# Performance work log

Measured on AMD Instinct MI355X. Metric: run time of the kernel, lower is better.

Reference implementation:

```python
import jax, jax.numpy as jnp
import numpy as np
from jax import lax

NUM_SEG = 64
EPS = 1e-12

def conv2d(x, w, b=None):
    y = lax.conv_general_dilated(x, w, (1, 1), 'SAME', dimension_numbers=('NCHW', 'OIHW', 'NCHW'))
    if b is not None:
        y = y + b[None, :, None, None]
    return y

def layer_norm_chw(x):
    # LayerNorm over (C,H,W) per sample, no affine
    mu = x.mean(axis=(1, 2, 3), keepdims=True)
    var = jnp.mean((x - mu) ** 2, axis=(1, 2, 3), keepdims=True)
    return (x - mu) / jnp.sqrt(var + EPS)

def spade(x, sem_rs, w_sh, b_sh, w_g, b_g, w_be, b_be):
    xn = layer_norm_chw(x)
    h = jax.nn.relu(conv2d(sem_rs, w_sh, b_sh))
    gamma = conv2d(h, w_g, b_g)
    beta = conv2d(h, w_be, b_be)
    return xn * (1.0 + gamma) + beta

def painted_semantic_map(f_sem, segmap):
    # f_sem: [B,C,Hp,Wp] float; segmap: [B,Hi,Wi] int
    B, C, Hp, Wp = f_sem.shape
    _, Hi, Wi = segmap.shape
    # torch nearest interpolate: src = floor(dst * in/out)
    rows = (jnp.arange(Hp) * Hi) // Hp
    cols = (jnp.arange(Wp) * Wi) // Wp
    seg_small = segmap[:, rows[:, None], cols[None, :]]  # [B,Hp,Wp]
    flat_feat = f_sem.transpose(0, 2, 3, 1).reshape(-1, C)  # [B*Hp*Wp, C]
    bidx = jnp.repeat(jnp.arange(B), Hp * Wp)
    gid = bidx * NUM_SEG + jnp.clip(seg_small.reshape(-1), 0, NUM_SEG - 1)
    sums = jax.ops.segment_sum(flat_feat, gid, num_segments=B * NUM_SEG)
    cnts = jax.ops.segment_sum(jnp.ones((flat_feat.shape[0],), flat_feat.dtype), gid, num_segments=B * NUM_SEG)
    # scatter_mean + nan_to_num: empty segments -> 0
    avg = jnp.where(cnts[:, None] > 0, sums / jnp.maximum(cnts, 1.0)[:, None], 0.0)
    pid = jnp.repeat(jnp.arange(B), Hi * Wi) * NUM_SEG + jnp.clip(segmap.reshape(-1), 0, NUM_SEG - 1)
    return avg[pid].reshape(B, Hi, Wi, C).transpose(0, 3, 1, 2)  # [B,C,Hi,Wi]

def setup_inputs() -> dict:
    key = jax.random.key(0)
    ks = jax.random.split(key, 32)
    B, Cm, Cs, Hp, Wp, Hi, Wi, Hm = 2, 1536, 384, 32, 32, 448, 448, 128
    d = {}
    d['x_main'] = jax.random.normal(ks[0], (B, Cm, Hp, Wp), jnp.float32)
    d['f_semantic'] = jax.random.normal(ks[1], (B, Cs, Hp, Wp), jnp.float32)
    s = 0.02
    d['w_sh0'] = jax.random.normal(ks[2], (Hm, Cs, 3, 3), jnp.float32) * s
    d['b_sh0'] = jax.random.normal(ks[3], (Hm,), jnp.float32) * s
    d['w_g0'] = jax.random.normal(ks[4], (Cm, Hm, 3, 3), jnp.float32) * s
    d['b_g0'] = jax.random.normal(ks[5], (Cm,), jnp.float32) * s
    d['w_be0'] = jax.random.normal(ks[6], (Cm, Hm, 3, 3), jnp.float32) * s
    d['b_be0'] = jax.random.normal(ks[7], (Cm,), jnp.float32) * s
    d['w_sh1'] = jax.random.normal(ks[8], (Hm, Cs, 3, 3), jnp.float32) * s
    d['b_sh1'] = jax.random.normal(ks[9], (Hm,), jnp.float32) * s
    d['w_g1'] = jax.random.normal(ks[10], (8, Hm, 3, 3), jnp.float32) * s
    d['b_g1'] = jax.random.normal(ks[11], (8,), jnp.float32) * s
    d['w_be1'] = jax.random.normal(ks[12], (8, Hm, 3, 3), jnp.float32) * s
    d['b_be1'] = jax.random.normal(ks[13], (8,), jnp.float32) * s
    d['w_sh2'] = jax.random.normal(ks[14], (Hm, Cs, 3, 3), jnp.float32) * s
    d['b_sh2'] = jax.random.normal(ks[15], (Hm,), jnp.float32) * s
    d['w_g2'] = jax.random.normal(ks[16], (16, Hm, 3, 3), jnp.float32) * s
    d['b_g2'] = jax.random.normal(ks[17], (16,), jnp.float32) * s
    d['w_be2'] = jax.random.normal(ks[18], (16, Hm, 3, 3), jnp.float32) * s
    d['b_be2'] = jax.random.normal(ks[19], (16,), jnp.float32) * s
    d['w_c0'] = jax.random.normal(ks[20], (8, Cm, 1, 1), jnp.float32) * s
    d['bias0'] = jax.random.normal(ks[21], (8,), jnp.float32) * s
    d['w_c1'] = jax.random.normal(ks[22], (16, 8, 1, 1), jnp.float32) * s
    d['bias1'] = jax.random.normal(ks[23], (16,), jnp.float32) * s
    d['w_c2'] = jax.random.normal(ks[24], (1, 16, 1, 1), jnp.float32) * s
    d['bias2'] = jax.random.normal(ks[25], (1,), jnp.float32) * s
    d['segmap'] = jax.random.randint(ks[26], (B, Hi, Wi), 0, NUM_SEG, jnp.int32)
    return d

def reference(x_main, f_semantic, w_sh0, b_sh0, w_g0, b_g0, w_be0, b_be0,
              w_sh1, b_sh1, w_g1, b_g1, w_be1, b_be1,
              w_sh2, b_sh2, w_g2, b_g2, w_be2, b_be2,
              w_c0, bias0, w_c1, bias1, w_c2, bias2, segmap):
    B, Cm, Hp, Wp = x_main.shape
    pm = painted_semantic_map(f_semantic, segmap)  # [B,Cs,Hi,Wi]
    # bilinear (align_corners=False) resize to main-path resolution; identical at all 3 SPADE layers
    sem_rs = jax.image.resize(pm, (B, pm.shape[1], Hp, Wp), method='bilinear')
    h = spade(x_main, sem_rs, w_sh0, b_sh0, w_g0, b_g0, w_be0, b_be0)
    h = jax.nn.softplus(conv2d(h, w_c0) + bias0[None, :, None, None])
    h = spade(h, sem_rs, w_sh1, b_sh1, w_g1, b_g1, w_be1, b_be1)
    h = jax.nn.softplus(conv2d(h, w_c1) + bias1[None, :, None, None])
    h = spade(h, sem_rs, w_sh2, b_sh2, w_g2, b_g2, w_be2, b_be2)
    h = jax.nn.softplus(conv2d(h, w_c2) + bias2[None, :, None, None])
    return h
```

## Files before the change

### kernel.cpp

```cpp
#include <hip/hip_runtime.h>
#include <hip/hip_bf16.h>

#define DEV __device__ __forceinline__

constexpr int B = 2;
constexpr int CM = 1536;
constexpr int CS = 384;
constexpr int HP = 32, WP = 32, P = 1024;
constexpr int HI = 448, WI = 448;
constexpr int HM = 128;
constexpr int NSEG = 64;

constexpr size_t OFF_AVG  = 0;
constexpr size_t OFF_SEMT = 49152;
constexpr size_t OFF_HSHT = 835584;
constexpr size_t OFF_OUT0 = 1622016;
constexpr size_t OFF_P6   = 4767744;
constexpr size_t OFF_H1A  = 5160960;
constexpr size_t OFF_OUT1 = 5177344;
constexpr size_t OFF_H2A  = 5193728;
constexpr size_t OFF_OUT2 = 5226496;
constexpr size_t OFF_STATS= 5259264;
constexpr size_t OFF_PACK = 5259280;

constexpr size_t PK0 = 0;
constexpr size_t PK1 = 1327104;
constexpr size_t PK2 = 4866048;
constexpr size_t PK3 = 4902912;
constexpr int    PK_CHUNKS = 617472;

typedef __attribute__((ext_vector_type(8))) short s16x8;
typedef __attribute__((ext_vector_type(4))) float f32x4;

DEV float softplus_f(float x) {
    return fmaxf(x, 0.f) + log1pf(expf(-fabsf(x)));
}
DEV ushort f2bf(float f) {
    union { float f; unsigned u; } x; x.f = f;
    unsigned r = x.u + 0x7fffu + ((x.u >> 16) & 1u);
    return (ushort)(r >> 16);
}
DEV float bf2f(ushort u) {
    union { unsigned u; float f; } x; x.u = ((unsigned)u) << 16;
    return x.f;
}

__global__ __launch_bounds__(256) void k_seg_avg(const float* __restrict__ f_sem,
                                                 const int* __restrict__ segmap,
                                                 float* __restrict__ ws) {
    int b = blockIdx.y;
    int c0 = blockIdx.x * 8;
    __shared__ int   segs[P];
    __shared__ float sums[NSEG][9];
    __shared__ float cnt[NSEG];
    int t = threadIdx.x;
    for (int i = t; i < NSEG * 9; i += 256) (&sums[0][0])[i] = 0.f;
    if (t < NSEG) cnt[t] = 0.f;
    __syncthreads();
    for (int p = t; p < P; p += 256) {
        int i = p >> 5, j = p & 31;
        int s = segmap[(b * HI + i * 14) * WI + j * 14];
        s = min(max(s, 0), NSEG - 1);
        segs[p] = s;
        atomicAdd(&cnt[s], 1.f);
    }
    __syncthreads();
    #pragma unroll
    for (int ch = 0; ch < 8; ++ch) {
        const float* fp = f_sem + ((size_t)b * CS + c0 + ch) * P;
        #pragma unroll
        for (int pb = 0; pb < 4; ++pb) {
            int p = pb * 256 + t;
            float v = fp[p];
            atomicAdd(&sums[segs[p]][ch], v);
        }
    }
    __syncthreads();
    for (int i = t; i < NSEG * 8; i += 256) {
        int s = i >> 3, ch = i & 7;
        float cv = cnt[s];
        ws[OFF_AVG + ((size_t)(b * NSEG + s)) * CS + c0 + ch] =
            cv > 0.f ? sums[s][ch] / cv : 0.f;
    }
}

__global__ __launch_bounds__(256) void k_paint(const int* __restrict__ segmap,
                                               float* __restrict__ ws) {
    int oxt = blockIdx.x, oy = blockIdx.y, b = blockIdx.z;
    int ox0 = oxt * 8;
    __shared__ float WbT[8][65];
    __shared__ float norm[8];
    int t = threadIdx.x;
    for (int i = t; i < 8 * 65; i += 256) (&WbT[0][0])[i] = 0.f;
    __syncthreads();

    float cy = 14.f * oy + 6.5f;
    int y0 = 14 * oy - 7;
    int x0 = 14 * ox0 - 7;
    for (int k = t; k < 28 * 126; k += 256) {
        int r = k / 126, cix = k % 126;
        int jy = y0 + r, jx = x0 + cix;
        if (jy < 0 || jy >= HI || jx < 0 || jx >= WI) continue;
        float wy = 1.f - fabsf(cy - (float)jy) * (1.f / 14.f);
        int s = segmap[(b * HI + jy) * WI + jx];
        s = min(max(s, 0), NSEG - 1);
        int oxhi = (jx + 7) / 14;
        #pragma unroll
        for (int d = 0; d < 2; ++d) {
            int ox = oxhi - d;
            if (ox < ox0 || ox >= ox0 + 8) continue;
            float wx = 1.f - fabsf(14.f * ox + 6.5f - (float)jx) * (1.f / 14.f);
            if (wx > 0.f) atomicAdd(&WbT[ox - ox0][s], wy * wx);
        }
    }
    __syncthreads();
    if (t < 8) {
        float sm = 0.f;
        #pragma unroll
        for (int s = 0; s < NSEG; ++s) sm += WbT[t][s];
        norm[t] = 1.f / sm;
    }
    __syncthreads();

    const float* ap0 = ws + OFF_AVG + (size_t)b * NSEG * CS;
    for (int c = t; c < CS; c += 256) {
        float acc[8] = {};
        const float* ap = ap0 + c;
        #pragma unroll
        for (int s = 0; s < NSEG; ++s) {
            float a = ap[(size_t)s * CS];
            #pragma unroll
            for (int ox = 0; ox < 8; ++ox) acc[ox] += WbT[ox][s] * a;
        }
        #pragma unroll
        for (int ox = 0; ox < 8; ++ox) {
            int op = oy * 32 + ox0 + ox;
            ws[OFF_SEMT + ((size_t)b * P + op) * CS + c] = acc[ox] * norm[ox];
        }
    }
}

__global__ __launch_bounds__(256) void k_ln0_stats(const float* __restrict__ x,
                                                   float* __restrict__ stats) {
    int b = blockIdx.y;
    const float4* xp = (const float4*)(x + (size_t)b * CM * P);
    int n4 = CM * P / 4;
    float s = 0.f, q = 0.f;
    for (int i = blockIdx.x * 256 + threadIdx.x; i < n4; i += 64 * 256) {
        float4 v = xp[i];
        s += v.x + v.y + v.z + v.w;
        q += v.x * v.x + v.y * v.y + v.z * v.z + v.w * v.w;
    }
    for (int o = 32; o > 0; o >>= 1) { s += __shfl_down(s, o); q += __shfl_down(q, o); }
    __shared__ float ls[4], lq[4];
    int w = threadIdx.x >> 6;
    if ((threadIdx.x & 63) == 0) { ls[w] = s; lq[w] = q; }
    __syncthreads();
    if (threadIdx.x == 0) {
        atomicAdd(&stats[b * 2],     ls[0] + ls[1] + ls[2] + ls[3]);
        atomicAdd(&stats[b * 2 + 1], lq[0] + lq[1] + lq[2] + lq[3]);
    }
}

__global__ __launch_bounds__(256) void k_wpack(
    const float* __restrict__ w_sh0, const float* __restrict__ w_sh1, const float* __restrict__ w_sh2,
    const float* __restrict__ w_g0,  const float* __restrict__ w_be0,
    const float* __restrict__ w_g1,  const float* __restrict__ w_be1,
    const float* __restrict__ w_g2,  const float* __restrict__ w_be2,
    ushort* __restrict__ packU)
{
    for (int c8 = blockIdx.x * 256 + threadIdx.x; c8 < PK_CHUNKS; c8 += gridDim.x * 256) {
        size_t e = (size_t)c8 * 8;
        const float* s0 = nullptr;
        bool zero = false;
        if (e < PK1) {
            size_t r = e;
            int ci0 = (int)(r & 31), co2 = (int)((r >> 5) & 31);
            int tap = (int)((r >> 10) % 9);
            int kct = (int)((r / 9216) % 12), ct = (int)(r / 110592);
            int coG = ct * 32 + co2, sel = coG >> 7, cow = coG & 127;
            const float* wp = sel == 0 ? w_sh0 : (sel == 1 ? w_sh1 : w_sh2);
            s0 = &wp[((size_t)cow * CS + kct * 32 + ci0) * 9 + tap];
        } else if (e < PK2) {
            size_t r = e - PK1;
            int ci0 = (int)(r & 31), co2 = (int)((r >> 5) & 31);
            int tap = (int)((r >> 10) % 9);
            int kct = (int)((r / 9216) % 4), ct = (int)(r / 36864);
            int cog = ct * 16 + (co2 & 15);
            const float* wp = co2 < 16 ? w_g0 : w_be0;
            s0 = &wp[((size_t)cog * HM + kct * 32 + ci0) * 9 + tap];
        } else if (e < PK3) {
            size_t r = e - PK2;
            int ci0 = (int)(r & 31), co2 = (int)((r >> 5) & 31);
            int tap = (int)((r >> 10) % 9);
            int kct = (int)(r / 9216);
            zero = ((co2 & 15) >= 8);
            int cog = co2 & 7;
            const float* wp = co2 < 16 ? w_g1 : w_be1;
            if (!zero) s0 = &wp[((size_t)cog * HM + kct * 32 + ci0) * 9 + tap];
        } else {
            size_t r = e - PK3;
            int ci0 = (int)(r & 31), co2 = (int)((r >> 5) & 31);
            int tap = (int)((r >> 10) % 9);
            int kct = (int)(r / 9216);
            int cog = co2 & 15;
            const float* wp = co2 < 16 ? w_g2 : w_be2;
            s0 = &wp[((size_t)cog * HM + kct * 32 + ci0) * 9 + tap];
        }
        s16x8 o;
        #pragma unroll
        for (int i = 0; i < 8; ++i) {
            float v = zero ? 0.f : s0[(size_t)i * 9];
            o[i] = (short)f2bf(v);
        }
        *(s16x8*)&packU[e] = o;
    }
}

template<int MODE>
__global__ __launch_bounds__(256) void k_conv_mfma(
    const float* __restrict__ semT, const ushort* __restrict__ hshTin,
    const ushort* __restrict__ packW,
    const float* __restrict__ bb0, const float* __restrict__ bb1, const float* __restrict__ bb2,
    const float* __restrict__ xsrc, const float* __restrict__ st, float Ninv,
    float* __restrict__ outF, ushort* __restrict__ outH)
{
    constexpr int ROWS = (MODE == 0) ? 4 : 8;
    constexpr int NT   = ROWS / 2;
    constexpr int XR   = ROWS + 2;
    constexpr int KTOT = (MODE == 0) ? 12 : 4;
    constexpr int CBASE = (MODE == 2) ? 128 : (MODE == 3) ? 256 : 0;
    constexpr int NP = (MODE == 1) ? 1536 : (MODE == 2) ? 8 : 16;

    int pt = blockIdx.x, ctile = blockIdx.y;
    int zz = blockIdx.z;
    int b  = (MODE == 0) ? (zz % B) : zz;
    int ks = (MODE == 0) ? (zz / B) : 0;
    int t = threadIdx.x, l = t & 63, wv = t >> 6;
    int y0 = pt * ROWS;

    __shared__ __align__(16) ushort Wl[9][32][40];
    __shared__ __align__(16) ushort Xl[XR][34][40];

    f32x4 acc[2][NT] = {};

    for (int kc = 0; kc < 128; kc += 32) {
        __syncthreads();
        for (int j = t; j < XR * 34 * 4; j += 256) {
            int slot = j >> 2, part = j & 3;
            int r = slot / 34, c = slot % 34;
            int gy = y0 - 1 + r, gx = c - 1;
            s16x8 v = {};
            if (gy >= 0 && gy < HP && gx >= 0 && gx < WP) {
                int pix = gy * WP + gx;
                if constexpr (MODE == 0) {
                    const float4* sp = (const float4*)&semT[((size_t)b * P + pix) * CS + ks * 128 + kc + part * 8];
                    float4 x0 = sp[0], x1 = sp[1];
                    v[0] = (short)f2bf(x0.x); v[1] = (short)f2bf(x0.y);
                    v[2] = (short)f2bf(x0.z); v[3] = (short)f2bf(x0.w);
                    v[4] = (short)f2bf(x1.x); v[5] = (short)f2bf(x1.y);
                    v[6] = (short)f2bf(x1.z); v[7] = (short)f2bf(x1.w);
                } else {
                    v = *(const s16x8*)&hshTin[((size_t)b * P + pix) * 384 + CBASE + kc + part * 8];
                }
            }
            *(s16x8*)&Xl[r][c][part * 8] = v;
        }
        const ushort* wsrc = packW + (size_t)(ctile * KTOT + ks * 4 + (kc >> 5)) * 9216;
        for (int j = t; j < 1152; j += 256) {
            int tap = j >> 7, co2 = (j >> 2) & 31, part = j & 3;
            *(s16x8*)&Wl[tap][co2][part * 8] = *(const s16x8*)&wsrc[(size_t)j * 8];
        }
        __syncthreads();
        #pragma unroll
        for (int tap = 0; tap < 9; ++tap) {
            int dy = tap / 3, dx = tap % 3;
            s16x8 a0 = *(const s16x8*)&Wl[tap][l & 15][(l >> 4) * 8];
            s16x8 a1 = *(const s16x8*)&Wl[tap][16 + (l & 15)][(l >> 4) * 8];
            #pragma unroll
            for (int nt = 0; nt < NT; ++nt) {
                int q = wv * (16 * NT) + nt * 16 + (l & 15);
                int ry = (q >> 5) + dy, rx = (q & 31) + dx;
                s16x8 bf = *(const s16x8*)&Xl[ry][rx][(l >> 4) * 8];
                acc[0][nt] = __builtin_amdgcn_mfma_f32_16x16x32_bf16(a0, bf, acc[0][nt], 0, 0, 0);
                acc[1][nt] = __builtin_amdgcn_mfma_f32_16x16x32_bf16(a1, bf, acc[1][nt], 0, 0, 0);
            }
        }
    }

    if constexpr (MODE == 0) {
        __syncthreads();
        ushort (*T)[36] = (ushort(*)[36])(&Xl[0][0][0]);
        #pragma unroll
        for (int mt = 0; mt < 2; ++mt)
            #pragma unroll
            for (int nt = 0; nt < NT; ++nt)
                #pragma unroll
                for (int r = 0; r < 4; ++r) {
                    int m = mt * 16 + (l >> 4) * 4 + r;
                    int pl = wv * (16 * NT) + nt * 16 + (l & 15);
                    T[pl][m] = f2bf(acc[mt][nt][r]);
                }
        __syncthreads();
        int row = t >> 1, half = t & 1;
        ushort* dst = outH + ((size_t)((ks * B + b) * P) + pt * 128 + row) * 384 + ctile * 32 + half * 16;
        *(s16x8*)dst = *(const s16x8*)&T[row][half * 16];
    } else {
        float mu = st[b * 2] * Ninv;
        float var = st[b * 2 + 1] * Ninv - mu * mu;
        float rs = rsqrtf(var + 1e-12f);
        #pragma unroll
        for (int nt = 0; nt < NT; ++nt)
            #pragma unroll
            for (int r = 0; r < 4; ++r) {
                int m = (l >> 4) * 4 + r;
                if (MODE == 2 && m >= 8) continue;
                int cog = (MODE == 1) ? ctile * 16 + m : m;
                int px = pt * 256 + wv * 64 + nt * 16 + (l & 15);
                float gam = acc[0][nt][r] + bb0[cog];
                float bet = acc[1][nt][r] + bb1[cog];
                float xv = xsrc[((size_t)b * NP + cog) * P + px];
                outF[((size_t)b * NP + cog) * P + px] = (xv - mu) * rs * (1.f + gam) + bet;
            }
    }
}

__global__ __launch_bounds__(256) void k_hsh_fin(const ushort* __restrict__ part,
                                                 const float* __restrict__ b0,
                                                 const float* __restrict__ b1,
                                                 const float* __restrict__ b2,
                                                 ushort* __restrict__ hsh) {
    int gid = blockIdx.x * 256 + threadIdx.x;
    int grp = gid % 48, pixg = gid / 48;
    int ch0 = grp * 8;
    size_t base = (size_t)pixg * 384 + ch0;
    s16x8 p0 = *(const s16x8*)&part[(size_t)0 * B * P * 384 + base];
    s16x8 p1 = *(const s16x8*)&part[(size_t)1 * B * P * 384 + base];
    s16x8 p2 = *(const s16x8*)&part[(size_t)2 * B * P * 384 + base];
    int sel = ch0 >> 7;
    const float* bp = sel == 0 ? b0 : (sel == 1 ? b1 : b2);
    int cb = ch0 & 127;
    s16x8 o;
    #pragma unroll
    for (int i = 0; i < 8; ++i) {
        float v = bf2f((ushort)p0[i]) + bf2f((ushort)p1[i]) + bf2f((ushort)p2[i]) + bp[cb + i];
        o[i] = (short)f2bf(fmaxf(v, 0.f));
    }
    *(s16x8*)&hsh[base] = o;
}

__global__ __launch_bounds__(256) void k_c1x1_a(const float* __restrict__ out0,
                                                const float* __restrict__ w,
                                                float* __restrict__ part) {
    int b = blockIdx.z, ks = blockIdx.y, pg = blockIdx.x;
    int t = threadIdx.x, lp = t & 63, g = t >> 6;
    int pix = pg * 64 + lp;
    float acc[8] = {};
    int ci0 = ks * 64 + g * 16;
    for (int i = 0; i < 16; i++) {
        int ci = ci0 + i;
        float v = out0[((size_t)b * CM + ci) * P + pix];
        #pragma unroll
        for (int o = 0; o < 8; o++) acc[o] += w[o * CM + ci] * v;
    }
    __shared__ float red[4][64][8];
    #pragma unroll
    for (int o = 0; o < 8; o++) red[g][lp][o] = acc[o];
    __syncthreads();
    for (int idx = t; idx < 512; idx += 256) {
        int pp = idx >> 3, o = idx & 7;
        float s = red[0][pp][o] + red[1][pp][o] + red[2][pp][o] + red[3][pp][o];
        part[(((size_t)b * 24 + ks) * 8 + o) * P + pg * 64 + pp] = s;
    }
}

__global__ __launch_bounds__(256) void k_c1x1_a_fin(const float* __restrict__ part,
                                                    const float* __restrict__ bias,
                                                    float* __restrict__ h1a,
                                                    float* __restrict__ stats) {
    int b = blockIdx.y, t = threadIdx.x;
    int idx = blockIdx.x * 1024 + t;
    float s = 0.f, q = 0.f;
    for (int k = 0; k < 4; ++k, idx += 256) {
        int o = idx >> 10, pix = idx & 1023;
        float v = 0.f;
        for (int ks = 0; ks < 24; ks++) v += part[(((size_t)b * 24 + ks) * 8 + o) * P + pix];
        v += bias[o];
        v = softplus_f(v);
        h1a[((size_t)b * 8 + o) * P + pix] = v;
        s += v; q += v * v;
    }
    for (int o2 = 32; o2 > 0; o2 >>= 1) { s += __shfl_down(s, o2); q += __shfl_down(q, o2); }
    __shared__ float ls[4], lq[4];
    int w = t >> 6;
    if ((t & 63) == 0) { ls[w] = s; lq[w] = q; }
    __syncthreads();
    if (t == 0) {
        atomicAdd(&stats[(B + b) * 2],     ls[0] + ls[1] + ls[2] + ls[3]);
        atomicAdd(&stats[(B + b) * 2 + 1], lq[0] + lq[1] + lq[2] + lq[3]);
    }
}

__global__ __launch_bounds__(256) void k_c1x1_b(const float* __restrict__ out1,
                                                const float* __restrict__ w,
                                                const float* __restrict__ bias,
                                                float* __restrict__ h2a,
                                                float* __restrict__ stats) {
    int b = blockIdx.y, t = threadIdx.x;
    int pix = blockIdx.x * 256 + t;
    float vin[8];
    #pragma unroll
    for (int ci = 0; ci < 8; ci++) vin[ci] = out1[((size_t)b * 8 + ci) * P + pix];
    float s = 0.f, q = 0.f;
    #pragma unroll
    for (int o = 0; o < 16; o++) {
        float a = bias[o];
        #pragma unroll
        for (int ci = 0; ci < 8; ci++) a += w[o * 8 + ci] * vin[ci];
        a = softplus_f(a);
        h2a[((size_t)b * 16 + o) * P + pix] = a;
        s += a; q += a * a;
    }
    for (int o2 = 32; o2 > 0; o2 >>= 1) { s += __shfl_down(s, o2); q += __shfl_down(q, o2); }
    __shared__ float ls[4], lq[4];
    int w2 = t >> 6;
    if ((t & 63) == 0) { ls[w2] = s; lq[w2] = q; }
    __syncthreads();
    if (t == 0) {
        atomicAdd(&stats[(2 * B + b) * 2],     ls[0] + ls[1] + ls[2] + ls[3]);
        atomicAdd(&stats[(2 * B + b) * 2 + 1], lq[0] + lq[1] + lq[2] + lq[3]);
    }
}

__global__ __launch_bounds__(256) void k_final(const float* __restrict__ out2,
                                               const float* __restrict__ w,
                                               const float* __restrict__ bias,
                                               float* __restrict__ out) {
    int b = blockIdx.y, t = threadIdx.x;
    int pix = blockIdx.x * 256 + t;
    float a = bias[0];
    #pragma unroll
    for (int ci = 0; ci < 16; ci++) a += w[ci] * out2[((size_t)b * 16 + ci) * P + pix];
    a = softplus_f(a);
    out[(size_t)b * P + pix] = a;
}

extern "C" void kernel_launch(void* const* d_in, const int* in_sizes, int n_in,
                              void* d_out, int out_size, void* d_ws, size_t ws_size,
                              hipStream_t stream) {
    const float* x_main = (const float*)d_in[0];
    const float* f_sem  = (const float*)d_in[1];
    const float* w_sh0 = (const float*)d_in[2];  const float* b_sh0 = (const float*)d_in[3];
    const float* w_g0  = (const float*)d_in[4];  const float* b_g0  = (const float*)d_in[5];
    const float* w_be0 = (const float*)d_in[6];  const float* b_be0 = (const float*)d_in[7];
    const float* w_sh1 = (const float*)d_in[8];  const float* b_sh1 = (const float*)d_in[9];
    const float* w_g1  = (const float*)d_in[10]; const float* b_g1  = (const float*)d_in[11];
    const float* w_be1 = (const float*)d_in[12]; const float* b_be1 = (const float*)d_in[13];
    const float* w_sh2 = (const float*)d_in[14]; const float* b_sh2 = (const float*)d_in[15];
    const float* w_g2  = (const float*)d_in[16]; const float* b_g2  = (const float*)d_in[17];
    const float* w_be2 = (const float*)d_in[18]; const float* b_be2 = (const float*)d_in[19];
    const float* w_c0  = (const float*)d_in[20]; const float* bias0 = (const float*)d_in[21];
    const float* w_c1  = (const float*)d_in[22]; const float* bias1 = (const float*)d_in[23];
    const float* w_c2  = (const float*)d_in[24]; const float* bias2 = (const float*)d_in[25];
    const int*   segmap = (const int*)d_in[26];

    float* ws = (float*)d_ws;
    float* out = (float*)d_out;
    float* stats = ws + OFF_STATS;
    ushort* hshU = (ushort*)(ws + OFF_HSHT);
    ushort* partU = (ushort*)(ws + OFF_OUT0);
    ushort* packU = (ushort*)(ws + OFF_PACK);

    hipMemsetAsync((void*)stats, 0, 16 * sizeof(float), stream);

    k_wpack<<<dim3(2412), 256, 0, stream>>>(w_sh0, w_sh1, w_sh2, w_g0, w_be0,
                                            w_g1, w_be1, w_g2, w_be2, packU);
    k_seg_avg<<<dim3(48, B), 256, 0, stream>>>(f_sem, segmap, ws);
    k_ln0_stats<<<dim3(64, B), 256, 0, stream>>>(x_main, stats);
    k_paint<<<dim3(4, 32, B), 256, 0, stream>>>(segmap, ws);

    k_conv_mfma<0><<<dim3(8, 12, 3 * B), 256, 0, stream>>>(
        ws + OFF_SEMT, nullptr, packU + PK0,
        nullptr, nullptr, nullptr, nullptr, nullptr, 0.f, nullptr, partU);
    k_hsh_fin<<<dim3(384), 256, 0, stream>>>(partU, b_sh0, b_sh1, b_sh2, hshU);

    k_conv_mfma<1><<<dim3(4, 96, B), 256, 0, stream>>>(
        nullptr, hshU, packU + PK1,
        b_g0, b_be0, nullptr, x_main, stats, 1.f / (float)(CM * P),
        ws + OFF_OUT0, nullptr);

    k_c1x1_a<<<dim3(16, 24, B), 256, 0, stream>>>(ws + OFF_OUT0, w_c0, ws + OFF_P6);
    k_c1x1_a_fin<<<dim3(8, B), 256, 0, stream>>>(ws + OFF_P6, bias0, ws + OFF_H1A, stats);

    k_conv_mfma<2><<<dim3(4, 1, B), 256, 0, stream>>>(
        nullptr, hshU, packU + PK2,
        b_g1, b_be1, nullptr, ws + OFF_H1A, stats + 2 * B, 1.f / (float)(8 * P),
        ws + OFF_OUT1, nullptr);

    k_c1x1_b<<<dim3(4, B), 256, 0, stream>>>(ws + OFF_OUT1, w_c1, bias1, ws + OFF_H2A, stats);

    k_conv_mfma<3><<<dim3(4, 1, B), 256, 0, stream>>>(
        nullptr, hshU, packU + PK3,
        b_g2, b_be2, nullptr, ws + OFF_H2A, stats + 4 * B, 1.f / (float)(16 * P),
        ws + OFF_OUT2, nullptr);

    k_final<<<dim3(4, B), 256, 0, stream>>>(ws + OFF_OUT2, w_c2, bias2, out);
}
```

Measured before the change: 319.4 us.

## Fuse 1x1 convs and softplus into SPADE conv epilogues

The SPADE-modulated output of each stage is no longer written to global memory. Instead, each conv kernel's epilogue applies the following 1x1 convolution directly. For stage 0, each channel tile writes per-tile partial sums of the 8 output channels, and a new finisher kernel reduces the 96 partials and applies softplus and the layer-norm stats. Stages 1 and 2 do their 1x1 conv, softplus and stats in-block through shared memory, which removes three kernel launches and the large fp32 intermediate round trip, at the cost of more epilogue work and a larger partial buffer.

```diff
diff --git a/kernel.cpp b/kernel.cpp
--- a/kernel.cpp
+++ b/kernel.cpp
@@ -221,9 +221,11 @@
 __global__ __launch_bounds__(256) void k_conv_mfma(
     const float* __restrict__ semT, const ushort* __restrict__ hshTin,
     const ushort* __restrict__ packW,
-    const float* __restrict__ bb0, const float* __restrict__ bb1, const float* __restrict__ bb2,
+    const float* __restrict__ bb0, const float* __restrict__ bb1,
     const float* __restrict__ xsrc, const float* __restrict__ st, float Ninv,
-    float* __restrict__ outF, ushort* __restrict__ outH)
+    const float* __restrict__ wcf, const float* __restrict__ bcf,
+    float* __restrict__ fout, float* __restrict__ statsOut,
+    ushort* __restrict__ outH)
 {
     constexpr int ROWS = (MODE == 0) ? 4 : 8;
     constexpr int NT   = ROWS / 2;
@@ -305,23 +307,104 @@
         int row = t >> 1, half = t & 1;
         ushort* dst = outH + ((size_t)((ks * B + b) * P) + pt * 128 + row) * 384 + ctile * 32 + half * 16;
         *(s16x8*)dst = *(const s16x8*)&T[row][half * 16];
+    } else if constexpr (MODE == 1) {
+        float mu = st[b * 2] * Ninv;
+        float var = st[b * 2 + 1] * Ninv - mu * mu;
+        float rs = rsqrtf(var + 1e-12f);
+        __syncthreads();
+        float (*WC)[17] = (float(*)[17])(&Wl[0][0][0]);
+        if (t < 128) WC[t >> 4][t & 15] = wcf[(size_t)(t >> 4) * CM + ctile * 16 + (t & 15)];
+        __syncthreads();
+        float pacc[8][4] = {};
+        #pragma unroll
+        for (int nt = 0; nt < NT; ++nt)
+            #pragma unroll
+            for (int r = 0; r < 4; ++r) {
+                int m = (l >> 4) * 4 + r;
+                int cog = ctile * 16 + m;
+                int px = pt * 256 + wv * 64 + nt * 16 + (l & 15);
+                float gam = acc[0][nt][r] + bb0[cog];
+                float bet = acc[1][nt][r] + bb1[cog];
+                float xv = xsrc[((size_t)b * NP + cog) * P + px];
+                float o0 = (xv - mu) * rs * (1.f + gam) + bet;
+                #pragma unroll
+                for (int o = 0; o < 8; ++o) pacc[o][nt] += WC[o][m] * o0;
+            }
+        #pragma unroll
+        for (int o = 0; o < 8; ++o)
+            #pragma unroll
+            for (int nt = 0; nt < NT; ++nt) {
+                float v = pacc[o][nt];
+                v += __shfl_xor(v, 16);
+                v += __shfl_xor(v, 32);
+                if ((l >> 4) == 0)
+                    fout[(((size_t)b * 96 + ctile) * 8 + o) * P + pt * 256 + wv * 64 + nt * 16 + l] = v;
+            }
+    } else if constexpr (MODE == 2) {
+        float mu = st[b * 2] * Ninv;
+        float var = st[b * 2 + 1] * Ninv - mu * mu;
+        float rs = rsqrtf(var + 1e-12f);
+        __syncthreads();
+        float (*O1)[9] = (float(*)[9])(&Xl[0][0][0]);
+        #pragma unroll
+        for (int nt = 0; nt < NT; ++nt)
+            #pragma unroll
+            for (int r = 0; r < 4; ++r) {
+                int m = (l >> 4) * 4 + r;
+                if (m < 8) {
+                    int pxl = wv * 64 + nt * 16 + (l & 15);
+                    int px = pt * 256 + pxl;
+                    float gam = acc[0][nt][r] + bb0[m];
+                    float bet = acc[1][nt][r] + bb1[m];
+                    float xv = xsrc[((size_t)b * NP + m) * P + px];
+                    O1[pxl][m] = (xv - mu) * rs * (1.f + gam) + bet;
+                }
+            }
+        __syncthreads();
+        float vin[8];
+        #pragma unroll
+        for (int ci = 0; ci < 8; ++ci) vin[ci] = O1[t][ci];
+        float s = 0.f, q = 0.f;
+        #pragma unroll
+        for (int o = 0; o < 16; ++o) {
+            float a = bcf[o];
+            #pragma unroll
+            for (int ci = 0; ci < 8; ++ci) a += wcf[o * 8 + ci] * vin[ci];
+            a = softplus_f(a);
+            fout[((size_t)b * 16 + o) * P + pt * 256 + t] = a;
+            s += a; q += a * a;
+        }
+        for (int o2 = 32; o2 > 0; o2 >>= 1) { s += __shfl_down(s, o2); q += __shfl_down(q, o2); }
+        float* red = (float*)&Wl[0][0][0];
+        if ((t & 63) == 0) { red[wv] = s; red[4 + wv] = q; }
+        __syncthreads();
+        if (t == 0) {
+            atomicAdd(&statsOut[b * 2],     red[0] + red[1] + red[2] + red[3]);
+            atomicAdd(&statsOut[b * 2 + 1], red[4] + red[5] + red[6] + red[7]);
+        }
     } else {
         float mu = st[b * 2] * Ninv;
         float var = st[b * 2 + 1] * Ninv - mu * mu;
         float rs = rsqrtf(var + 1e-12f);
+        __syncthreads();
+        float (*O2)[17] = (float(*)[17])(&Xl[0][0][0]);
         #pragma unroll
         for (int nt = 0; nt < NT; ++nt)
             #pragma unroll
             for (int r = 0; r < 4; ++r) {
                 int m = (l >> 4) * 4 + r;
-                if (MODE == 2 && m >= 8) continue;
-                int cog = (MODE == 1) ? ctile * 16 + m : m;
-                int px = pt * 256 + wv * 64 + nt * 16 + (l & 15);
-                float gam = acc[0][nt][r] + bb0[cog];
-                float bet = acc[1][nt][r] + bb1[cog];
-                float xv = xsrc[((size_t)b * NP + cog) * P + px];
-                outF[((size_t)b * NP + cog) * P + px] = (xv - mu) * rs * (1.f + gam) + bet;
+                int pxl = wv * 64 + nt * 16 + (l & 15);
+                int px = pt * 256 + pxl;
+                float gam = acc[0][nt][r] + bb0[m];
+                float bet = acc[1][nt][r] + bb1[m];
+                float xv = xsrc[((size_t)b * NP + m) * P + px];
+                O2[pxl][m] = (xv - mu) * rs * (1.f + gam) + bet;
             }
+        __syncthreads();
+        float a = bcf[0];
+        #pragma unroll
+        for (int ci = 0; ci < 16; ++ci) a += wcf[ci] * O2[t][ci];
+        fout[(size_t)b * P + pt * 256 + t] = softplus_f(a);
     }
 }
 
@@ -349,47 +432,21 @@
     *(s16x8*)&hsh[base] = o;
 }
 
-__global__ __launch_bounds__(256) void k_c1x1_a(const float* __restrict__ out0,
-                                                const float* __restrict__ w,
-                                                float* __restrict__ part) {
-    int b = blockIdx.z, ks = blockIdx.y, pg = blockIdx.x;
-    int t = threadIdx.x, lp = t & 63, g = t >> 6;
-    int pix = pg * 64 + lp;
-    float acc[8] = {};
-    int ci0 = ks * 64 + g * 16;
-    for (int i = 0; i < 16; i++) {
-        int ci = ci0 + i;
-        float v = out0[((size_t)b * CM + ci) * P + pix];
-        #pragma unroll
-        for (int o = 0; o < 8; o++) acc[o] += w[o * CM + ci] * v;
-    }
-    __shared__ float red[4][64][8];
-    #pragma unroll
-    for (int o = 0; o < 8; o++) red[g][lp][o] = acc[o];
-    __syncthreads();
-    for (int idx = t; idx < 512; idx += 256) {
-        int pp = idx >> 3, o = idx & 7;
-        float s = red[0][pp][o] + red[1][pp][o] + red[2][pp][o] + red[3][pp][o];
-        part[(((size_t)b * 24 + ks) * 8 + o) * P + pg * 64 + pp] = s;
-    }
-}
-
-__global__ __launch_bounds__(256) void k_c1x1_a_fin(const float* __restrict__ part,
-                                                    const float* __restrict__ bias,
-                                                    float* __restrict__ h1a,
-                                                    float* __restrict__ stats) {
+__global__ __launch_bounds__(256) void k_c1a_fin(const float* __restrict__ part,
+                                                 const float* __restrict__ bias,
+                                                 float* __restrict__ h1a,
+                                                 float* __restrict__ stats) {
     int b = blockIdx.y, t = threadIdx.x;
-    int idx = blockIdx.x * 1024 + t;
-    float s = 0.f, q = 0.f;
-    for (int k = 0; k < 4; ++k, idx += 256) {
-        int o = idx >> 10, pix = idx & 1023;
-        float v = 0.f;
-        for (int ks = 0; ks < 24; ks++) v += part[(((size_t)b * 24 + ks) * 8 + o) * P + pix];
-        v += bias[o];
-        v = softplus_f(v);
-        h1a[((size_t)b * 8 + o) * P + pix] = v;
-        s += v; q += v * v;
-    }
+    int idx = blockIdx.x * 256 + t;
+    int o = idx >> 10, pix = idx & 1023;
+    float v = 0.f;
+    #pragma unroll 8
+    for (int ct = 0; ct < 96; ++ct)
+        v += part[(((size_t)b * 96 + ct) * 8 + o) * P + pix];
+    v += bias[o];
+    v = softplus_f(v);
+    h1a[((size_t)b * 8 + o) * P + pix] = v;
+    float s = v, q = v * v;
     for (int o2 = 32; o2 > 0; o2 >>= 1) { s += __shfl_down(s, o2); q += __shfl_down(q, o2); }
     __shared__ float ls[4], lq[4];
     int w = t >> 6;
@@ -399,50 +456,6 @@
         atomicAdd(&stats[(B + b) * 2],     ls[0] + ls[1] + ls[2] + ls[3]);
         atomicAdd(&stats[(B + b) * 2 + 1], lq[0] + lq[1] + lq[2] + lq[3]);
     }
-}
-
-__global__ __launch_bounds__(256) void k_c1x1_b(const float* __restrict__ out1,
-                                                const float* __restrict__ w,
-                                                const float* __restrict__ bias,
-                                                float* __restrict__ h2a,
-                                                float* __restrict__ stats) {
-    int b = blockIdx.y, t = threadIdx.x;
-    int pix = blockIdx.x * 256 + t;
-    float vin[8];
-    #pragma unroll
-    for (int ci = 0; ci < 8; ci++) vin[ci] = out1[((size_t)b * 8 + ci) * P + pix];
-    float s = 0.f, q = 0.f;
-    #pragma unroll
-    for (int o = 0; o < 16; o++) {
-        float a = bias[o];
-        #pragma unroll
-        for (int ci = 0; ci < 8; ci++) a += w[o * 8 + ci] * vin[ci];
-        a = softplus_f(a);
-        h2a[((size_t)b * 16 + o) * P + pix] = a;
-        s += a; q += a * a;
-    }
-    for (int o2 = 32; o2 > 0; o2 >>= 1) { s += __shfl_down(s, o2); q += __shfl_down(q, o2); }
-    __shared__ float ls[4], lq[4];
-    int w2 = t >> 6;
-    if ((t & 63) == 0) { ls[w2] = s; lq[w2] = q; }
-    __syncthreads();
-    if (t == 0) {
-        atomicAdd(&stats[(2 * B + b) * 2],     ls[0] + ls[1] + ls[2] + ls[3]);
-        atomicAdd(&stats[(2 * B + b) * 2 + 1], lq[0] + lq[1] + lq[2] + lq[3]);
-    }
-}
-
-__global__ __launch_bounds__(256) void k_final(const float* __restrict__ out2,
-                                               const float* __restrict__ w,
-                                               const float* __restrict__ bias,
-                                               float* __restrict__ out) {
-    int b = blockIdx.y, t = threadIdx.x;
-    int pix = blockIdx.x * 256 + t;
-    float a = bias[0];
-    #pragma unroll
-    for (int ci = 0; ci < 16; ci++) a += w[ci] * out2[((size_t)b * 16 + ci) * P + pix];
-    a = softplus_f(a);
-    out[(size_t)b * P + pix] = a;
 }
 
 extern "C" void kernel_launch(void* const* d_in, const int* in_sizes, int n_in,
@@ -469,6 +482,7 @@
     float* stats = ws + OFF_STATS;
     ushort* hshU = (ushort*)(ws + OFF_HSHT);
     ushort* partU = (ushort*)(ws + OFF_OUT0);
+    float*  partA = ws + OFF_OUT0;
     ushort* packU = (ushort*)(ws + OFF_PACK);
 
     hipMemsetAsync((void*)stats, 0, 16 * sizeof(float), stream);
@@ -481,28 +495,23 @@
 
     k_conv_mfma<0><<<dim3(8, 12, 3 * B), 256, 0, stream>>>(
         ws + OFF_SEMT, nullptr, packU + PK0,
-        nullptr, nullptr, nullptr, nullptr, nullptr, 0.f, nullptr, partU);
+        nullptr, nullptr, nullptr, nullptr, 0.f,
+        nullptr, nullptr, nullptr, nullptr, partU);
     k_hsh_fin<<<dim3(384), 256, 0, stream>>>(partU, b_sh0, b_sh1, b_sh2, hshU);
 
     k_conv_mfma<1><<<dim3(4, 96, B), 256, 0, stream>>>(
         nullptr, hshU, packU + PK1,
-        b_g0, b_be0, nullptr, x_main, stats, 1.f / (float)(CM * P),
-        ws + OFF_OUT0, nullptr);
-
-    k_c1x1_a<<<dim3(16, 24, B), 256, 0, stream>>>(ws + OFF_OUT0, w_c0, ws + OFF_P6);
-    k_c1x1_a_fin<<<dim3(8, B), 256, 0, stream>>>(ws + OFF_P6, bias0, ws + OFF_H1A, stats);
+        b_g0, b_be0, x_main, stats, 1.f / (float)(CM * P),
+        w_c0, nullptr, partA, nullptr, nullptr);
+    k_c1a_fin<<<dim3(32, B), 256, 0, stream>>>(partA, bias0, ws + OFF_H1A, stats);
 
     k_conv_mfma<2><<<dim3(4, 1, B), 256, 0, stream>>>(
         nullptr, hshU, packU + PK2,
-        b_g1, b_be1, nullptr, ws + OFF_H1A, stats + 2 * B, 1.f / (float)(8 * P),
-        ws + OFF_OUT1, nullptr);
-
-    k_c1x1_b<<<dim3(4, B), 256, 0, stream>>>(ws + OFF_OUT1, w_c1, bias1, ws + OFF_H2A, stats);
+        b_g1, b_be1, ws + OFF_H1A, stats + 2 * B, 1.f / (float)(8 * P),
+        w_c1, bias1, ws + OFF_H2A, stats + 4 * B, nullptr);
 
     k_conv_mfma<3><<<dim3(4, 1, B), 256, 0, stream>>>(
         nullptr, hshU, packU + PK3,
-        b_g2, b_be2, nullptr, ws + OFF_H2A, stats + 4 * B, 1.f / (float)(16 * P),
-        ws + OFF_OUT2, nullptr);
-
-    k_final<<<dim3(4, B), 256, 0, stream>>>(ws + OFF_OUT2, w_c2, bias2, out);
-}
+        b_g2, b_be2, ws + OFF_H2A, stats + 4 * B, 1.f / (float)(16 * P),
+        w_c2, bias2, out, nullptr, nullptr);
+}
```

Result: faster. 306.4 us (-4.1%).
